# Performance work log

Measured on AMD Instinct MI355X. Metric: run time of the kernel, lower is better.

The kernel has to match this reference:

```python
import jax, jax.numpy as jnp
import numpy as np

B, T, D = 32, 4096, 256          # batch, seq_len, input_dim
H = 64                           # CausalEventModel hidden (hard-coded in __init__)
A = D + 3                        # anchor_dim = input_dim + 3
K_DIM = 256                      # lift output dim (k_dim)
D_MODEL = 1024                   # topology_proj output dim
MAX_PROXY = 16                   # max_proxy_points


def setup_inputs() -> dict:
    key = jax.random.key(0)
    ks = jax.random.split(key, 6)
    def w(k, shape, fan):
        return jax.random.normal(k, shape, jnp.float32) * (1.0 / np.sqrt(fan))
    return {
        "x": jax.random.normal(ks[0], (B, T, D), jnp.float32),
        # CausalEventModel: 2-layer MLP scorer -> event_scores [B,T]
        "W1": w(ks[1], (D, H), D), "b1": jnp.zeros((H,), jnp.float32),
        "W2": w(ks[2], (H, 1), H), "b2": jnp.zeros((1,), jnp.float32),
        # NormalizedLift: (v-mu)/sigma then tanh(Linear(anchor_dim->k_dim))
        "Wl": w(ks[3], (A, K_DIM), A), "bl": jnp.zeros((K_DIM,), jnp.float32),
        "mu": jnp.zeros((A,), jnp.float32), "sigma": jnp.ones((A,), jnp.float32),
        # topology_proj: Linear(k_dim -> d_model)
        "Wp": w(ks[4], (K_DIM, D_MODEL), K_DIM), "bp": jnp.zeros((D_MODEL,), jnp.float32),
    }


def reference(x, W1, b1, W2, b2, Wl, bl, mu, sigma, Wp, bp):
    # --- event model: per-timestep saliency scores [B, T] ---
    h = jax.nn.relu(jnp.einsum("btd,dh->bth", x, W1) + b1)
    event_scores = (jnp.einsum("bth,ho->bto", h, W2) + b2)[..., 0]
    sal = jax.nn.sigmoid(event_scores)                     # saliency_scores [B, T]
    Bn, Tn = sal.shape

    # --- uniform index selection + one-hot scatter ---
    k_eff = min(Tn, MAX_PROXY)
    idx = jnp.linspace(0.0, Tn - 1, k_eff).astype(jnp.int32)   # [K_eff]
    y_star = jnp.zeros((Bn, Tn), x.dtype).at[:, idx].set(1.0)  # scatter_ ones

    # --- dense anchor vectors: concat(x, saliency, time, cum-saliency) [B,T,D+3] ---
    t_norm = jnp.broadcast_to((jnp.arange(Tn, dtype=x.dtype) / Tn)[None, :, None],
                              (Bn, Tn, 1))
    cum = (jnp.cumsum(sal, axis=1) / Tn)[..., None]
    anchors = jnp.concatenate([x, sal[..., None], t_norm, cum], axis=-1)

    # --- topology projection: L2-normalize onto unit sphere ---
    v = anchors / (jnp.linalg.norm(anchors, axis=-1, keepdims=True) + 1e-6)

    # --- NormalizedLift over the FULL dense sequence (the wasted compute) ---
    z = (v - mu) / sigma
    lifted = jnp.tanh(jnp.einsum("bta,ak->btk", z, Wl) + bl)   # [B, T, K_DIM]

    # --- gather K_eff positions, then final projection ---
    cloud = lifted[:, idx, :]                                  # [B, K_eff, K_DIM]
    tokens = jnp.einsum("bkc,cm->bkm", cloud, Wp) + bp         # [B, K_eff, D_MODEL]
    return tokens, y_star
```

## Files before the change

### kernel.cpp

```cpp
#include <hip/hip_runtime.h>
#include <hip/hip_bf16.h>
#include <math.h>

#define B_ 32
#define T_ 4096
#define D_ 256
#define H_ 64
#define A_ 259
#define K_ 256
#define M_ 1024
#define P_ 16
#define STEP_ 273

typedef __attribute__((ext_vector_type(8))) short bf16x8;
typedef __attribute__((ext_vector_type(4))) float f32x4;

__device__ __forceinline__ short f32_to_bf16_rne(float f) {
    unsigned u = __builtin_bit_cast(unsigned, f);
    unsigned r = (u + 0x7fffu + ((u >> 16) & 1u)) >> 16;
    return (short)r;
}

__global__ __launch_bounds__(256, 4) void k1_sal(
    const float* __restrict__ x, const float* __restrict__ W1,
    const float* __restrict__ b1, const float* __restrict__ W2,
    const float* __restrict__ b2, float* __restrict__ sal)
{
    __shared__ short w1f[8][4][64 * 8];
    const int tid = threadIdx.x;

    #pragma unroll
    for (int i = 0; i < 8; ++i) {
        const int e = tid + i * 256;
        const int lane = e & 63;
        const int ktnt = e >> 6;
        const int kt = ktnt >> 2, nt = ktnt & 3;
        const int n  = nt * 16 + (lane & 15);
        const int k0 = kt * 32 + (lane >> 4) * 8;
        bf16x8 v;
        #pragma unroll
        for (int j = 0; j < 8; ++j)
            v[j] = f32_to_bf16_rne(W1[(size_t)(k0 + j) * H_ + n]);
        *(bf16x8*)&w1f[kt][nt][lane * 8] = v;
    }
    __syncthreads();

    const int wave = tid >> 6, lane = tid & 63;
    const int m = lane & 15, q = lane >> 4;
    const int row0 = blockIdx.x * 128;

    #pragma unroll 1
    for (int g = 0; g < 2; ++g) {
        const int rowbase = row0 + g * 64 + wave * 16;
        const float* xrow = x + (size_t)(rowbase + m) * D_ + q * 8;

        float4 xb[16];
        #pragma unroll
        for (int kt = 0; kt < 8; ++kt) {
            xb[2 * kt]     = *(const float4*)(xrow + kt * 32);
            xb[2 * kt + 1] = *(const float4*)(xrow + kt * 32 + 4);
        }

        f32x4 acc[4] = {{0,0,0,0},{0,0,0,0},{0,0,0,0},{0,0,0,0}};
        #pragma unroll
        for (int kt = 0; kt < 8; ++kt) {
            const float4 p0 = xb[2 * kt], p1 = xb[2 * kt + 1];
            bf16x8 a;
            a[0] = f32_to_bf16_rne(p0.x); a[1] = f32_to_bf16_rne(p0.y);
            a[2] = f32_to_bf16_rne(p0.z); a[3] = f32_to_bf16_rne(p0.w);
            a[4] = f32_to_bf16_rne(p1.x); a[5] = f32_to_bf16_rne(p1.y);
            a[6] = f32_to_bf16_rne(p1.z); a[7] = f32_to_bf16_rne(p1.w);
            #pragma unroll
            for (int nt = 0; nt < 4; ++nt) {
                const bf16x8 bfr = *(const bf16x8*)&w1f[kt][nt][lane * 8];
                acc[nt] = __builtin_amdgcn_mfma_f32_16x16x32_bf16(a, bfr, acc[nt], 0, 0, 0);
            }
        }

        float part[4];
        #pragma unroll
        for (int reg = 0; reg < 4; ++reg) {
            float s = 0.f;
            #pragma unroll
            for (int nt = 0; nt < 4; ++nt) {
                const int n = nt * 16 + m;
                const float hv = acc[nt][reg] + b1[n];
                s = fmaf(fmaxf(hv, 0.f), W2[n], s);
            }
            part[reg] = s;
        }
        #pragma unroll
        for (int off = 1; off < 16; off <<= 1) {
            #pragma unroll
            for (int reg = 0; reg < 4; ++reg)
                part[reg] += __shfl_xor(part[reg], off, 64);
        }
        const int r3 = m & 3;
        const float myv = (r3 == 0) ? part[0] : (r3 == 1) ? part[1]
                        : (r3 == 2) ? part[2] : part[3];
        if (m < 4) {
            const float score = myv + b2[0];
            sal[rowbase + q * 4 + m] = 1.f / (1.f + __expf(-score));
        }
    }
}

__global__ __launch_bounds__(256) void k2_scan(
    const float* __restrict__ sal, float* __restrict__ cumsel,
    float* __restrict__ ystar)
{
    const int tid = threadIdx.x;

    {
        const int g = blockIdx.x * 256 + tid;
        const int ty = g & (T_ - 1);
        ystar[g] = ((ty % STEP_) == 0) ? 1.f : 0.f;
    }

    const int b = blockIdx.x >> 4, i = blockIdx.x & 15;
    const int len = STEP_ * i + 1;
    const float* sp = sal + (size_t)b * T_;
    float s = 0.f;
    for (int t = tid; t < len; t += 256) s += sp[t];

    #pragma unroll
    for (int off = 32; off > 0; off >>= 1) s += __shfl_xor(s, off, 64);
    __shared__ float red[4];
    if ((tid & 63) == 0) red[tid >> 6] = s;
    __syncthreads();
    if (tid == 0)
        cumsel[b * P_ + i] = (red[0] + red[1] + red[2] + red[3]) * (1.0f / (float)T_);
}

__global__ __launch_bounds__(256) void k3a_lift(
    const float* __restrict__ x, const float* __restrict__ sal,
    const float* __restrict__ cumsel, const float* __restrict__ Wl,
    const float* __restrict__ bl, const float* __restrict__ mu,
    const float* __restrict__ sigma, float* __restrict__ lift)
{
    __shared__ float z[4][260];
    __shared__ float part[4 * 4 * 256];
    const int tid = threadIdx.x;
    const int wave = tid >> 6, lane = tid & 63;

    {
        const int r = wave;
        const int s = blockIdx.x * 4 + r;
        const int b = s >> 4, i = s & 15;
        const int pos = STEP_ * i;
        const float* xrow = x + ((size_t)b * T_ + pos) * D_;
        const float4 xv = *(const float4*)(xrow + 4 * lane);
        const float sv = sal[b * T_ + pos];
        const float tn = (float)pos * (1.0f / (float)T_);
        const float cv = cumsel[b * P_ + i];

        float p = xv.x*xv.x + xv.y*xv.y + xv.z*xv.z + xv.w*xv.w;
        #pragma unroll
        for (int off = 32; off > 0; off >>= 1) p += __shfl_xor(p, off, 64);
        const float ss = p + sv * sv + tn * tn + cv * cv;
        const float inv = 1.0f / (sqrtf(ss) + 1e-6f);

        const float4 muv = *(const float4*)(mu + 4 * lane);
        const float4 sgv = *(const float4*)(sigma + 4 * lane);
        z[r][4*lane+0] = (xv.x * inv - muv.x) / sgv.x;
        z[r][4*lane+1] = (xv.y * inv - muv.y) / sgv.y;
        z[r][4*lane+2] = (xv.z * inv - muv.z) / sgv.z;
        z[r][4*lane+3] = (xv.w * inv - muv.w) / sgv.w;
        if (lane < 3) {
            const float e = (lane == 0) ? sv : (lane == 1) ? tn : cv;
            z[r][256 + lane] = (e * inv - mu[256 + lane]) / sigma[256 + lane];
        }
    }
    __syncthreads();

    const int a0 = wave * 65;
    const int a1 = (wave == 3) ? A_ : a0 + 65;
    f32x4 acc[4] = {{0,0,0,0},{0,0,0,0},{0,0,0,0},{0,0,0,0}};
    const float4* Wl4 = (const float4*)Wl;

    #pragma unroll 4
    for (int a = a0; a < a1; ++a) {
        const float4 wv = Wl4[a * 64 + lane];
        #pragma unroll
        for (int r = 0; r < 4; ++r) {
            const float zv = z[r][a];
            acc[r][0] = fmaf(zv, wv.x, acc[r][0]);
            acc[r][1] = fmaf(zv, wv.y, acc[r][1]);
            acc[r][2] = fmaf(zv, wv.z, acc[r][2]);
            acc[r][3] = fmaf(zv, wv.w, acc[r][3]);
        }
    }
    {
        f32x4* p4 = (f32x4*)part;
        #pragma unroll
        for (int r = 0; r < 4; ++r)
            p4[(wave * 4 + r) * 64 + lane] = acc[r];
    }
    __syncthreads();

    const int r = tid >> 6;
    const size_t base = (size_t)blockIdx.x * 4 * K_;
    #pragma unroll
    for (int j = 0; j < 4; ++j) {
        const int k = lane + 64 * j;
        float val = bl[k];
        #pragma unroll
        for (int w = 0; w < 4; ++w)
            val += part[(w * 4 + r) * 256 + k];
        lift[base + r * K_ + k] = tanhf(val);
    }
}

__global__ __launch_bounds__(256) void k3b_tok(
    const float* __restrict__ lift, const float* __restrict__ Wp,
    const float* __restrict__ bp, float* __restrict__ tokens)
{
    __shared__ float ls[8 * K_];
    __shared__ float part[4 * 8 * 256];
    const int tid = threadIdx.x;
    const int wave = tid >> 6, lane = tid & 63;
    const int mt = blockIdx.x & 3;
    const int rh = (blockIdx.x >> 2) & 1;
    const int b  = blockIdx.x >> 3;
    const int s0 = b * P_ + rh * 8;
    const int m0 = mt * 256;

    const float4* lg = (const float4*)(lift + (size_t)s0 * K_);
    float4* lsl = (float4*)ls;
    lsl[tid] = lg[tid];
    lsl[tid + 256] = lg[tid + 256];
    __syncthreads();

    f32x4 acc[8] = {{0,0,0,0},{0,0,0,0},{0,0,0,0},{0,0,0,0},
                    {0,0,0,0},{0,0,0,0},{0,0,0,0},{0,0,0,0}};
    const float4* Wp4 = (const float4*)(Wp + m0);

    #pragma unroll 2
    for (int c4 = 0; c4 < 16; ++c4) {
        const int c = wave * 64 + c4 * 4;
        float4 lsv[8];
        #pragma unroll
        for (int r = 0; r < 8; ++r)
            lsv[r] = *(const float4*)&ls[r * K_ + c];
        #pragma unroll
        for (int cc = 0; cc < 4; ++cc) {
            const float4 wv = Wp4[(size_t)(c + cc) * 256 + lane];
            #pragma unroll
            for (int r = 0; r < 8; ++r) {
                const float lv = (cc == 0) ? lsv[r].x : (cc == 1) ? lsv[r].y
                               : (cc == 2) ? lsv[r].z : lsv[r].w;
                acc[r][0] = fmaf(lv, wv.x, acc[r][0]);
                acc[r][1] = fmaf(lv, wv.y, acc[r][1]);
                acc[r][2] = fmaf(lv, wv.z, acc[r][2]);
                acc[r][3] = fmaf(lv, wv.w, acc[r][3]);
            }
        }
    }
    {
        f32x4* p4 = (f32x4*)part;
        #pragma unroll
        for (int r = 0; r < 8; ++r)
            p4[(wave * 8 + r) * 64 + lane] = acc[r];
    }
    __syncthreads();

    const float bv = bp[m0 + tid];
    #pragma unroll
    for (int r = 0; r < 8; ++r) {
        float val = bv;
        #pragma unroll
        for (int w = 0; w < 4; ++w)
            val += part[(w * 8 + r) * 256 + tid];
        tokens[(size_t)(s0 + r) * M_ + m0 + tid] = val;
    }
}

extern "C" void kernel_launch(void* const* d_in, const int* in_sizes, int n_in,
                              void* d_out, int out_size, void* d_ws, size_t ws_size,
                              hipStream_t stream)
{
    (void)in_sizes; (void)n_in; (void)out_size; (void)ws_size;
    const float* x  = (const float*)d_in[0];
    const float* W1 = (const float*)d_in[1];
    const float* b1 = (const float*)d_in[2];
    const float* W2 = (const float*)d_in[3];
    const float* b2 = (const float*)d_in[4];
    const float* Wl = (const float*)d_in[5];
    const float* bl = (const float*)d_in[6];
    const float* mu = (const float*)d_in[7];
    const float* sg = (const float*)d_in[8];
    const float* Wp = (const float*)d_in[9];
    const float* bp = (const float*)d_in[10];

    float* out    = (float*)d_out;
    float* tokens = out;
    float* ystar  = out + (size_t)B_ * P_ * M_;

    float* ws     = (float*)d_ws;
    float* sal    = ws;
    float* cumsel = ws + (size_t)B_ * T_;
    float* lift   = cumsel + B_ * P_;

    k1_sal<<<dim3((B_ * T_) / 128), dim3(256), 0, stream>>>(x, W1, b1, W2, b2, sal);
    k2_scan<<<dim3(B_ * P_), dim3(256), 0, stream>>>(sal, cumsel, ystar);
    k3a_lift<<<dim3((B_ * P_) / 4), dim3(256), 0, stream>>>(x, sal, cumsel, Wl, bl, mu, sg, lift);
    k3b_tok<<<dim3(B_ * 2 * 4), dim3(256), 0, stream>>>(lift, Wp, bp, tokens);
}
```

Before: 269.4 us.

## Keep W1 fragments in registers and stage x tiles via direct global-to-LDS loads

The saliency kernel now loads each wave's W1 bf16 fragments directly into registers, which removes the shared-memory W1 staging and its barrier. The x rows are copied into a padded LDS tile with global_load_lds and then read back as MFMA operands. Each block now processes 256 rows in four tiles instead of 128 rows, and occupancy is lowered to 2 blocks per SM. This is meant to cut redundant W1 conversion work and improve load efficiency on the memory-bound x read. In exchange it adds register pressure and a full vmcnt wait per tile with no overlap between loads and compute, and it is unclear whether each wave reads only the LDS rows it wrote itself without a barrier.

```diff
diff --git a/kernel.cpp b/kernel.cpp
--- a/kernel.cpp
+++ b/kernel.cpp
@@ -12,6 +12,8 @@
 #define P_ 16
 #define STEP_ 273
 
+#define XSTRIDE 260
+
 typedef __attribute__((ext_vector_type(8))) short bf16x8;
 typedef __attribute__((ext_vector_type(4))) float f32x4;
 
@@ -21,60 +23,69 @@
     return (short)r;
 }
 
-__global__ __launch_bounds__(256, 4) void k1_sal(
+__global__ __launch_bounds__(256, 2) void k1_sal(
     const float* __restrict__ x, const float* __restrict__ W1,
     const float* __restrict__ b1, const float* __restrict__ W2,
     const float* __restrict__ b2, float* __restrict__ sal)
 {
-    __shared__ short w1f[8][4][64 * 8];
+    __shared__ float xt[64 * XSTRIDE];
     const int tid = threadIdx.x;
-
-    #pragma unroll
-    for (int i = 0; i < 8; ++i) {
-        const int e = tid + i * 256;
-        const int lane = e & 63;
-        const int ktnt = e >> 6;
-        const int kt = ktnt >> 2, nt = ktnt & 3;
-        const int n  = nt * 16 + (lane & 15);
-        const int k0 = kt * 32 + (lane >> 4) * 8;
-        bf16x8 v;
-        #pragma unroll
-        for (int j = 0; j < 8; ++j)
-            v[j] = f32_to_bf16_rne(W1[(size_t)(k0 + j) * H_ + n]);
-        *(bf16x8*)&w1f[kt][nt][lane * 8] = v;
-    }
-    __syncthreads();
-
     const int wave = tid >> 6, lane = tid & 63;
     const int m = lane & 15, q = lane >> 4;
-    const int row0 = blockIdx.x * 128;
+
+    bf16x8 bfr[8][4];
+    #pragma unroll
+    for (int kt = 0; kt < 8; ++kt) {
+        #pragma unroll
+        for (int nt = 0; nt < 4; ++nt) {
+            const int n  = nt * 16 + m;
+            const int k0 = kt * 32 + q * 8;
+            bf16x8 v;
+            #pragma unroll
+            for (int j = 0; j < 8; ++j)
+                v[j] = f32_to_bf16_rne(W1[(k0 + j) * H_ + n]);
+            bfr[kt][nt] = v;
+        }
+    }
+    float b1v[4], w2v[4];
+    #pragma unroll
+    for (int nt = 0; nt < 4; ++nt) {
+        b1v[nt] = b1[nt * 16 + m];
+        w2v[nt] = W2[nt * 16 + m];
+    }
+    const float b2s = b2[0];
+
+    const int row0 = blockIdx.x * 256;
+    const int rl = wave * 16;
 
     #pragma unroll 1
-    for (int g = 0; g < 2; ++g) {
-        const int rowbase = row0 + g * 64 + wave * 16;
-        const float* xrow = x + (size_t)(rowbase + m) * D_ + q * 8;
-
-        float4 xb[16];
+    for (int t = 0; t < 4; ++t) {
+        const int tilebase = row0 + t * 64;
+
+        #pragma unroll
+        for (int j = 0; j < 16; ++j) {
+            const float* gsrc = x + (size_t)(tilebase + rl + j) * D_ + lane * 4;
+            __builtin_amdgcn_global_load_lds(
+                (const __attribute__((address_space(1))) unsigned int*)gsrc,
+                (__attribute__((address_space(3))) unsigned int*)&xt[(rl + j) * XSTRIDE],
+                16, 0, 0);
+        }
+        __asm__ volatile("s_waitcnt vmcnt(0)" ::: "memory");
+
+        f32x4 acc[4] = {{0,0,0,0},{0,0,0,0},{0,0,0,0},{0,0,0,0}};
+        const int abase = (rl + m) * XSTRIDE + q * 8;
         #pragma unroll
         for (int kt = 0; kt < 8; ++kt) {
-            xb[2 * kt]     = *(const float4*)(xrow + kt * 32);
-            xb[2 * kt + 1] = *(const float4*)(xrow + kt * 32 + 4);
-        }
-
-        f32x4 acc[4] = {{0,0,0,0},{0,0,0,0},{0,0,0,0},{0,0,0,0}};
-        #pragma unroll
-        for (int kt = 0; kt < 8; ++kt) {
-            const float4 p0 = xb[2 * kt], p1 = xb[2 * kt + 1];
+            const float4 p0 = *(const float4*)&xt[abase + kt * 32];
+            const float4 p1 = *(const float4*)&xt[abase + kt * 32 + 4];
             bf16x8 a;
             a[0] = f32_to_bf16_rne(p0.x); a[1] = f32_to_bf16_rne(p0.y);
             a[2] = f32_to_bf16_rne(p0.z); a[3] = f32_to_bf16_rne(p0.w);
             a[4] = f32_to_bf16_rne(p1.x); a[5] = f32_to_bf16_rne(p1.y);
             a[6] = f32_to_bf16_rne(p1.z); a[7] = f32_to_bf16_rne(p1.w);
             #pragma unroll
-            for (int nt = 0; nt < 4; ++nt) {
-                const bf16x8 bfr = *(const bf16x8*)&w1f[kt][nt][lane * 8];
-                acc[nt] = __builtin_amdgcn_mfma_f32_16x16x32_bf16(a, bfr, acc[nt], 0, 0, 0);
-            }
+            for (int nt = 0; nt < 4; ++nt)
+                acc[nt] = __builtin_amdgcn_mfma_f32_16x16x32_bf16(a, bfr[kt][nt], acc[nt], 0, 0, 0);
         }
 
         float part[4];
@@ -83,9 +94,8 @@
             float s = 0.f;
             #pragma unroll
             for (int nt = 0; nt < 4; ++nt) {
-                const int n = nt * 16 + m;
-                const float hv = acc[nt][reg] + b1[n];
-                s = fmaf(fmaxf(hv, 0.f), W2[n], s);
+                const float hv = acc[nt][reg] + b1v[nt];
+                s = fmaf(fmaxf(hv, 0.f), w2v[nt], s);
             }
             part[reg] = s;
         }
@@ -99,8 +109,8 @@
         const float myv = (r3 == 0) ? part[0] : (r3 == 1) ? part[1]
                         : (r3 == 2) ? part[2] : part[3];
         if (m < 4) {
-            const float score = myv + b2[0];
-            sal[rowbase + q * 4 + m] = 1.f / (1.f + __expf(-score));
+            const float score = myv + b2s;
+            sal[tilebase + rl + q * 4 + m] = 1.f / (1.f + __expf(-score));
         }
     }
 }
@@ -301,7 +311,7 @@
     float* cumsel = ws + (size_t)B_ * T_;
     float* lift   = cumsel + B_ * P_;
 
-    k1_sal<<<dim3((B_ * T_) / 128), dim3(256), 0, stream>>>(x, W1, b1, W2, b2, sal);
+    k1_sal<<<dim3((B_ * T_) / 256), dim3(256), 0, stream>>>(x, W1, b1, W2, b2, sal);
     k2_scan<<<dim3(B_ * P_), dim3(256), 0, stream>>>(sal, cumsel, ystar);
     k3a_lift<<<dim3((B_ * P_) / 4), dim3(256), 0, stream>>>(x, sal, cumsel, Wl, bl, mu, sg, lift);
     k3b_tok<<<dim3(B_ * 2 * 4), dim3(256), 0, stream>>>(lift, Wp, bp, tokens);
```

New measurement: 256.9 us. 1.05x faster.
